# Kernel tuning notes

Measured on AMD Instinct MI355X. Metric: run time of the kernel, lower is better.

Reference implementation:

```python
import jax, jax.numpy as jnp
import numpy as np

SEQ, BATCH, IN_DIM, HID = 1024, 256, 256, 256


def setup_inputs() -> dict:
    key = jax.random.key(0)
    ks = jax.random.split(key, 9)
    s = 1.0 / np.sqrt(IN_DIM + HID)
    inp = {
        "inputs": jax.random.normal(ks[0], (SEQ, BATCH, IN_DIM), dtype=jnp.float32),
        "h0": jnp.zeros((BATCH, HID), dtype=jnp.float32),
        "c0": jnp.zeros((BATCH, HID), dtype=jnp.float32),
        # torch nn.Linear weights: [out, in] with y = x @ W.T + b
        "Wf": jax.random.uniform(ks[1], (HID, IN_DIM + HID), jnp.float32, -s, s),
        "bf": jax.random.uniform(ks[2], (HID,), jnp.float32, -s, s),
        "Wi": jax.random.uniform(ks[3], (HID, IN_DIM + HID), jnp.float32, -s, s),
        "bi": jax.random.uniform(ks[4], (HID,), jnp.float32, -s, s),
        "Wg": jax.random.uniform(ks[5], (HID, IN_DIM + HID), jnp.float32, -s, s),
        "bg": jax.random.uniform(ks[6], (HID,), jnp.float32, -s, s),
        "Wo": jax.random.uniform(ks[7], (HID, IN_DIM + HID), jnp.float32, -s, s),
        "bo": jax.random.uniform(ks[8], (HID,), jnp.float32, -s, s),
    }
    return inp


def reference(inputs, h0, c0, Wf, bf, Wi, bi, Wg, bg, Wo, bo):
    # inputs: [S, B, I]; recurrence over S via lax.scan
    def step(carry, x):
        hx, cx = carry
        combined = jnp.concatenate([x, hx], axis=1)  # [B, I+H]
        f = jax.nn.sigmoid(combined @ Wf.T + bf)
        i = jax.nn.sigmoid(combined @ Wi.T + bi)
        g = jnp.tanh(combined @ Wg.T + bg)
        o = jax.nn.sigmoid(combined @ Wo.T + bo)
        cx = f * cx + i * g
        hx = o * jnp.tanh(cx)
        return (hx, cx), hx

    (hx, cx), stacked = jax.lax.scan(step, (h0, c0), inputs)
    return stacked, (hx, cx)
```

## Files before the change

### kernel.cpp

```cpp
#include <hip/hip_runtime.h>
#include <hip/hip_bf16.h>
#include <math.h>

#define SEQ   1024
#define BATCH 256
#define IND   256
#define HID   256
#define NGATE 4

#define WB_BYTES   (2 * NGATE * HID * 256 * 2)
#define REG_BYTES  512

typedef float  f32x4  __attribute__((ext_vector_type(4)));
typedef short  bf16x8 __attribute__((ext_vector_type(8)));
typedef unsigned long long u64;

__device__ __forceinline__ short f2bf(float x) {
    __hip_bfloat16 h = __float2bfloat16(x);
    return *reinterpret_cast<short*>(&h);
}

__device__ __forceinline__ bf16x8 pack8(const float4& a, const float4& b) {
    union { short sh[8]; bf16x8 v; } u;
    u.sh[0] = f2bf(a.x); u.sh[1] = f2bf(a.y); u.sh[2] = f2bf(a.z); u.sh[3] = f2bf(a.w);
    u.sh[4] = f2bf(b.x); u.sh[5] = f2bf(b.y); u.sh[6] = f2bf(b.z); u.sh[7] = f2bf(b.w);
    return u.v;
}

__device__ __forceinline__ void gload_lds16(const void* g, void* l) {
    __builtin_amdgcn_global_load_lds(
        (const __attribute__((address_space(1))) unsigned int*)g,
        (__attribute__((address_space(3))) unsigned int*)l, 16, 0, 0);
}

__device__ __forceinline__ float sigmoid_f(float z) {
    return 1.f / (1.f + __expf(-z));
}
__device__ __forceinline__ float tanh_f(float v) {
    return 2.f / (1.f + __expf(-2.f * v)) - 1.f;
}

__device__ __forceinline__ bool stamp_ok(u64 q0, u64 q1, u64 ee) {
    return ((((q0 ^ ee) | (q1 ^ ee)) & 1ULL) == 0ULL);
}


__global__ __launch_bounds__(256) void prep_w(
    const float* __restrict__ Wf, const float* __restrict__ Wi,
    const float* __restrict__ Wg, const float* __restrict__ Wo,
    unsigned char* __restrict__ wb)
{
    int chunk = blockIdx.x * 256 + threadIdx.x;
    int g  = chunk >> 14;
    int jj = (chunk >> 6) & 255;
    int k0 = (chunk & 63) * 8;
    int p  = k0 >> 8;
    int kk = k0 & 255;
    const float* W = (g == 0) ? Wf : (g == 1) ? Wi : (g == 2) ? Wg : Wo;
    const float* src = W + (size_t)jj * 512 + k0;
    float4 a = *reinterpret_cast<const float4*>(src);
    float4 b = *reinterpret_cast<const float4*>(src + 4);
    size_t dstrow = (size_t)((p * 4 + g) * 256 + jj);
    *reinterpret_cast<bf16x8*>(
        wb + dstrow * 512 + ((kk * 2) ^ ((jj & 7) << 4))) = pack8(a, b);
}

__global__ __launch_bounds__(256) void prep_h0(
    const float* __restrict__ h0, unsigned char* __restrict__ hr)
{
    int idx  = blockIdx.x * 256 + threadIdx.x;
    int slot = idx >> 14;
    int g    = (idx >> 10) & 15;
    int J    = (idx >> 6) & 15;
    int c    = idx & 63;
    int br   = c >> 2;
    int j4   = (c & 3) * 4;
    const float* src = h0 + (size_t)(g * 16 + br) * HID + J * 16 + j4;
    unsigned short v[4];
    #pragma unroll
    for (int i = 0; i < 4; ++i)
        v[i] = (unsigned short)((unsigned short)f2bf(src[i]) | 1u);
    u64 q = (u64)v[0] | ((u64)v[1] << 16) | ((u64)v[2] << 32) | ((u64)v[3] << 48);
    *reinterpret_cast<u64*>(
        hr + (size_t)((slot * 16 + g) * 16 + J) * REG_BYTES + c * 8) = q;
}

__global__ __launch_bounds__(64, 1) void lstm_seq(
    const float* __restrict__ x,  const float* __restrict__ c0,
    const float* __restrict__ bf_, const float* __restrict__ bi_,
    const float* __restrict__ bg_, const float* __restrict__ bo_,
    const unsigned char* __restrict__ wb, unsigned char* __restrict__ hr,
    float* __restrict__ out, float* __restrict__ hx, float* __restrict__ cxg)
{
    extern __shared__ __align__(16) unsigned char smem[];

    const int lane = threadIdx.x & 63;
    const int blk  = blockIdx.x;
    const int g_   = blk & 15;
    const int J    = blk >> 4;
    const int j0   = J * 16;
    const int b0   = g_ * 16;

    const int lrow = lane & 15;
    const int hi   = lane >> 4;
    const int j    = j0 + lrow;

    #pragma unroll
    for (int i = 0; i < 64; ++i) {
        gload_lds16(wb + ((size_t)((i >> 3) * 256 + j0 + (i & 7) * 2)) * 512
                       + lane * 16,
                    smem + i * 1024);
    }
    const float biasF = bf_[j], biasI = bi_[j], biasG = bg_[j], biasO = bo_[j];
    float cst[4];
    #pragma unroll
    for (int r = 0; r < 4; ++r)
        cst[r] = c0[(b0 + hi * 4 + r) * HID + j];
    __syncthreads();

    const int bswz = (lrow & 7) << 4;
    bf16x8 wf[2][8][4];
    #pragma unroll
    for (int p = 0; p < 2; ++p) {
        #pragma unroll
        for (int kc = 0; kc < 8; ++kc) {
            int wbyte = (kc * 64 + hi * 16) ^ bswz;
            #pragma unroll
            for (int gg = 0; gg < 4; ++gg)
                wf[p][kc][gg] = *reinterpret_cast<const bf16x8*>(
                    smem + p * 32768 + gg * 8192 + lrow * 512 + wbyte);
        }
    }

    float4 xt0[8], xt1[8];
    bf16x8 xpk[8];
    {
        const float* xr = x + (size_t)(b0 + lrow) * IND;
        #pragma unroll
        for (int kc = 0; kc < 8; ++kc) {
            const float* p = xr + kc * 32 + hi * 8;
            xt0[kc] = *reinterpret_cast<const float4*>(p);
            xt1[kc] = *reinterpret_cast<const float4*>(p + 4);
        }
        #pragma unroll
        for (int kc = 0; kc < 8; ++kc) xpk[kc] = pack8(xt0[kc], xt1[kc]);
        const float* xr1 = x + ((size_t)BATCH + b0 + lrow) * IND;
        #pragma unroll
        for (int kc = 0; kc < 8; ++kc) {
            const float* p = xr1 + kc * 32 + hi * 8;
            xt0[kc] = *reinterpret_cast<const float4*>(p);
            xt1[kc] = *reinterpret_cast<const float4*>(p + 4);
        }
    }

    unsigned char* regc[2] = {
        hr + (size_t)((0 * 16 + g_) * 16) * REG_BYTES,
        hr + (size_t)((1 * 16 + g_) * 16) * REG_BYTES };
    unsigned char* regp[2] = { regc[0] + J * REG_BYTES, regc[1] + J * REG_BYTES };

    for (int s = 0; s < SEQ; ++s) {
        const u64 ee = (u64)(((unsigned)(s + 3) >> 1) & 1);
        const unsigned char* hsrc = regc[s & 1];

        u64 hq0[8], hq1[8];
        #pragma unroll
        for (int kc = 0; kc < 8; ++kc) {
            const u64* p = reinterpret_cast<const u64*>(
                hsrc + (2 * kc + (hi >> 1)) * REG_BYTES + lrow * 32 + (hi & 1) * 16);
            hq0[kc] = __hip_atomic_load(p,     __ATOMIC_RELAXED, __HIP_MEMORY_SCOPE_AGENT);
            hq1[kc] = __hip_atomic_load(p + 1, __ATOMIC_RELAXED, __HIP_MEMORY_SCOPE_AGENT);
        }
        __builtin_amdgcn_sched_barrier(0);

        f32x4 aF = {0.f, 0.f, 0.f, 0.f};
        f32x4 aI = {0.f, 0.f, 0.f, 0.f};
        f32x4 aG = {0.f, 0.f, 0.f, 0.f};
        f32x4 aO = {0.f, 0.f, 0.f, 0.f};
        #pragma unroll
        for (int kc = 0; kc < 8; ++kc) {
            aF = __builtin_amdgcn_mfma_f32_16x16x32_bf16(xpk[kc], wf[0][kc][0], aF, 0, 0, 0);
            aI = __builtin_amdgcn_mfma_f32_16x16x32_bf16(xpk[kc], wf[0][kc][1], aI, 0, 0, 0);
            aG = __builtin_amdgcn_mfma_f32_16x16x32_bf16(xpk[kc], wf[0][kc][2], aG, 0, 0, 0);
            aO = __builtin_amdgcn_mfma_f32_16x16x32_bf16(xpk[kc], wf[0][kc][3], aO, 0, 0, 0);
        }

        #pragma unroll
        for (int kc = 0; kc < 8; ++kc) xpk[kc] = pack8(xt0[kc], xt1[kc]);
        if (s + 2 < SEQ) {
            const float* xr = x + ((size_t)(s + 2) * BATCH + b0 + lrow) * IND;
            #pragma unroll
            for (int kc = 0; kc < 8; ++kc) {
                const float* p = xr + kc * 32 + hi * 8;
                xt0[kc] = *reinterpret_cast<const float4*>(p);
                xt1[kc] = *reinterpret_cast<const float4*>(p + 4);
            }
        }
        __builtin_amdgcn_sched_barrier(0);

        #pragma unroll
        for (int half = 0; half < 2; ++half) {
            const int kb = half * 4;
            unsigned pend = 0;
            #pragma unroll
            for (int kc = 0; kc < 4; ++kc)
                if (!stamp_ok(hq0[kb + kc], hq1[kb + kc], ee)) pend |= (1u << kc);
            while (pend) {
                #pragma unroll
                for (int kc = 0; kc < 4; ++kc) {
                    if (pend & (1u << kc)) {
                        const u64* p = reinterpret_cast<const u64*>(
                            hsrc + (2 * (kb + kc) + (hi >> 1)) * REG_BYTES
                                 + lrow * 32 + (hi & 1) * 16);
                        hq0[kb + kc] = __hip_atomic_load(p,     __ATOMIC_RELAXED, __HIP_MEMORY_SCOPE_AGENT);
                        hq1[kb + kc] = __hip_atomic_load(p + 1, __ATOMIC_RELAXED, __HIP_MEMORY_SCOPE_AGENT);
                        if (stamp_ok(hq0[kb + kc], hq1[kb + kc], ee)) pend &= ~(1u << kc);
                    }
                }
            }
            #pragma unroll
            for (int kc = 0; kc < 4; ++kc) {
                union { u64 q[2]; bf16x8 v; } u;
                u.q[0] = hq0[kb + kc]; u.q[1] = hq1[kb + kc];
                aF = __builtin_amdgcn_mfma_f32_16x16x32_bf16(u.v, wf[1][kb + kc][0], aF, 0, 0, 0);
                aI = __builtin_amdgcn_mfma_f32_16x16x32_bf16(u.v, wf[1][kb + kc][1], aI, 0, 0, 0);
                aG = __builtin_amdgcn_mfma_f32_16x16x32_bf16(u.v, wf[1][kb + kc][2], aG, 0, 0, 0);
                aO = __builtin_amdgcn_mfma_f32_16x16x32_bf16(u.v, wf[1][kb + kc][3], aO, 0, 0, 0);
            }
        }

        float hv[4];
        #pragma unroll
        for (int r = 0; r < 4; ++r) {
            float fg = sigmoid_f(aF[r] + biasF);
            float ig = sigmoid_f(aI[r] + biasI);
            float gg = tanh_f(aG[r] + biasG);
            float og = sigmoid_f(aO[r] + biasO);
            cst[r] = fg * cst[r] + ig * gg;
            hv[r]  = og * tanh_f(cst[r]);
        }
        #pragma unroll
        for (int r = 0; r < 4; ++r) {
            int bl = hi * 4 + r;
            *reinterpret_cast<short*>(smem + bl * 32 + lrow * 2) = f2bf(hv[r]);
            *reinterpret_cast<float*>(smem + 512 + bl * 64 + lrow * 4) = hv[r];
        }
        __builtin_amdgcn_sched_barrier(0);
        asm volatile("s_waitcnt lgkmcnt(0)" ::: "memory");
        __builtin_amdgcn_sched_barrier(0);

        {
            u64 w = *reinterpret_cast<const u64*>(smem + lane * 8);
            w = (w & ~1ULL) | (u64)((s >> 1) & 1);
            __hip_atomic_store(
                reinterpret_cast<u64*>(regp[(s + 1) & 1] + lane * 8),
                w, __ATOMIC_RELAXED, __HIP_MEMORY_SCOPE_AGENT);
        }
        {
            float4 ov = *reinterpret_cast<const float4*>(smem + 512 + lane * 16);
            *reinterpret_cast<float4*>(
                out + (size_t)s * (BATCH * HID)
                    + (size_t)(b0 + (lane >> 2)) * HID + j0 + (lane & 3) * 4) = ov;
        }
        if (s == SEQ - 1) {
            #pragma unroll
            for (int r = 0; r < 4; ++r) {
                int gi = (b0 + hi * 4 + r) * HID + j;
                hx[gi] = hv[r]; cxg[gi] = cst[r];
            }
        }
    }
}

extern "C" void kernel_launch(void* const* d_in, const int* in_sizes, int n_in,
                              void* d_out, int out_size, void* d_ws, size_t ws_size,
                              hipStream_t stream) {
    const float* x  = (const float*)d_in[0];
    const float* h0 = (const float*)d_in[1];
    const float* c0 = (const float*)d_in[2];
    const float* Wf = (const float*)d_in[3];
    const float* bf = (const float*)d_in[4];
    const float* Wi = (const float*)d_in[5];
    const float* bi = (const float*)d_in[6];
    const float* Wg = (const float*)d_in[7];
    const float* bg = (const float*)d_in[8];
    const float* Wo = (const float*)d_in[9];
    const float* bo = (const float*)d_in[10];

    float* out = (float*)d_out;
    float* hx  = out + (size_t)SEQ * BATCH * HID;
    float* cx  = hx + BATCH * HID;

    unsigned char* wb = (unsigned char*)d_ws;
    unsigned char* hr = wb + WB_BYTES;

    prep_w<<<256, 256, 0, stream>>>(Wf, Wi, Wg, Wo, wb);
    prep_h0<<<128, 256, 0, stream>>>(h0, hr);
    lstm_seq<<<256, 64, 65536, stream>>>(x, c0, bf, bi, bg, bo,
                                         wb, hr, out, hx, cx);
}
```

Baseline: 2.502 ms.

## Add producer wavefront that polls remote h state into LDS for compute wave

Adds a second wavefront per block that spins on the global stamped h buffers and copies validated chunks into a double-buffered LDS region, then signals the compute wave with an LDS flag. The compute wave now waits on the local flag and reads h from LDS instead of polling global memory itself, and it defers the fp32 output store by one step so that store overlaps the next step's work. It also raises the compute wave's priority. This is meant to take global polling latency off the critical recurrence path. The cost is an extra wave per CU and an LDS-flag handoff that relies on volatile ordering without a barrier.

```diff
diff --git a/kernel.cpp b/kernel.cpp
--- a/kernel.cpp
+++ b/kernel.cpp
@@ -10,6 +10,11 @@
 
 #define WB_BYTES   (2 * NGATE * HID * 256 * 2)
 #define REG_BYTES  512
+
+#define HBUF_OFF   0
+#define FLAG_OFF   16384
+#define HST_OFF    16448
+#define OST_OFF    17024
 
 typedef float  f32x4  __attribute__((ext_vector_type(4)));
 typedef short  bf16x8 __attribute__((ext_vector_type(8)));
@@ -85,7 +90,7 @@
         hr + (size_t)((slot * 16 + g) * 16 + J) * REG_BYTES + c * 8) = q;
 }
 
-__global__ __launch_bounds__(64, 1) void lstm_seq(
+__global__ __launch_bounds__(128, 1) void lstm_seq(
     const float* __restrict__ x,  const float* __restrict__ c0,
     const float* __restrict__ bf_, const float* __restrict__ bi_,
     const float* __restrict__ bg_, const float* __restrict__ bo_,
@@ -94,7 +99,9 @@
 {
     extern __shared__ __align__(16) unsigned char smem[];
 
-    const int lane = threadIdx.x & 63;
+    const int tid  = threadIdx.x;
+    const int lane = tid & 63;
+    const int w    = tid >> 6;
     const int blk  = blockIdx.x;
     const int g_   = blk & 15;
     const int J    = blk >> 4;
@@ -106,31 +113,87 @@
     const int j    = j0 + lrow;
 
     #pragma unroll
-    for (int i = 0; i < 64; ++i) {
-        gload_lds16(wb + ((size_t)((i >> 3) * 256 + j0 + (i & 7) * 2)) * 512
+    for (int i = 0; i < 32; ++i) {
+        int idx = w * 32 + i;
+        gload_lds16(wb + ((size_t)((idx >> 3) * 256 + j0 + (idx & 7) * 2)) * 512
                        + lane * 16,
-                    smem + i * 1024);
-    }
+                    smem + idx * 1024);
+    }
+    __syncthreads();
+
+    const int bswz = (lrow & 7) << 4;
+    bf16x8 wf[2][8][4];
+    if (w == 0) {
+        #pragma unroll
+        for (int p = 0; p < 2; ++p) {
+            #pragma unroll
+            for (int kc = 0; kc < 8; ++kc) {
+                int wbyte = (kc * 64 + hi * 16) ^ bswz;
+                #pragma unroll
+                for (int gg = 0; gg < 4; ++gg)
+                    wf[p][kc][gg] = *reinterpret_cast<const bf16x8*>(
+                        smem + p * 32768 + gg * 8192 + lrow * 512 + wbyte);
+            }
+        }
+    }
+    __syncthreads();
+    if (tid == 0) *(volatile int*)(smem + FLAG_OFF) = 0;
+    __syncthreads();
+
+    unsigned char* regc[2] = {
+        hr + (size_t)((0 * 16 + g_) * 16) * REG_BYTES,
+        hr + (size_t)((1 * 16 + g_) * 16) * REG_BYTES };
+
+    if (w == 1) {
+        for (int s = 0; s < SEQ; ++s) {
+            const u64 ee = (u64)(((unsigned)(s + 3) >> 1) & 1);
+            const unsigned char* hsrc = regc[s & 1];
+            unsigned char* dst = smem + HBUF_OFF + (s & 1) * 8192 + lane * 16;
+
+            u64 qa0[8], qa1[8];
+            #pragma unroll
+            for (int kc = 0; kc < 8; ++kc) {
+                const u64* p = reinterpret_cast<const u64*>(
+                    hsrc + (2 * kc + (hi >> 1)) * REG_BYTES + lrow * 32 + (hi & 1) * 16);
+                qa0[kc] = __hip_atomic_load(p,     __ATOMIC_RELAXED, __HIP_MEMORY_SCOPE_AGENT);
+                qa1[kc] = __hip_atomic_load(p + 1, __ATOMIC_RELAXED, __HIP_MEMORY_SCOPE_AGENT);
+            }
+            unsigned done = 0;
+            while (done != 0xffu) {
+                u64 qb0[8], qb1[8];
+                #pragma unroll
+                for (int kc = 0; kc < 8; ++kc) {
+                    const u64* p = reinterpret_cast<const u64*>(
+                        hsrc + (2 * kc + (hi >> 1)) * REG_BYTES + lrow * 32 + (hi & 1) * 16);
+                    qb0[kc] = __hip_atomic_load(p,     __ATOMIC_RELAXED, __HIP_MEMORY_SCOPE_AGENT);
+                    qb1[kc] = __hip_atomic_load(p + 1, __ATOMIC_RELAXED, __HIP_MEMORY_SCOPE_AGENT);
+                }
+                #pragma unroll
+                for (int kc = 0; kc < 8; ++kc) {
+                    if (!((done >> kc) & 1) && stamp_ok(qa0[kc], qa1[kc], ee)) {
+                        union { u64 q[2]; bf16x8 v; } u;
+                        u.q[0] = qa0[kc]; u.q[1] = qa1[kc];
+                        *reinterpret_cast<bf16x8*>(dst + kc * 1024) = u.v;
+                        done |= (1u << kc);
+                    }
+                }
+                #pragma unroll
+                for (int kc = 0; kc < 8; ++kc) { qa0[kc] = qb0[kc]; qa1[kc] = qb1[kc]; }
+            }
+            __builtin_amdgcn_sched_barrier(0);
+            asm volatile("s_waitcnt lgkmcnt(0)" ::: "memory");
+            if (lane == 0) *(volatile int*)(smem + FLAG_OFF) = s + 1;
+        }
+        return;
+    }
+
+    __builtin_amdgcn_s_setprio(1);
+
     const float biasF = bf_[j], biasI = bi_[j], biasG = bg_[j], biasO = bo_[j];
     float cst[4];
     #pragma unroll
     for (int r = 0; r < 4; ++r)
         cst[r] = c0[(b0 + hi * 4 + r) * HID + j];
-    __syncthreads();
-
-    const int bswz = (lrow & 7) << 4;
-    bf16x8 wf[2][8][4];
-    #pragma unroll
-    for (int p = 0; p < 2; ++p) {
-        #pragma unroll
-        for (int kc = 0; kc < 8; ++kc) {
-            int wbyte = (kc * 64 + hi * 16) ^ bswz;
-            #pragma unroll
-            for (int gg = 0; gg < 4; ++gg)
-                wf[p][kc][gg] = *reinterpret_cast<const bf16x8*>(
-                    smem + p * 32768 + gg * 8192 + lrow * 512 + wbyte);
-        }
-    }
 
     float4 xt0[8], xt1[8];
     bf16x8 xpk[8];
@@ -153,25 +216,11 @@
         }
     }
 
-    unsigned char* regc[2] = {
-        hr + (size_t)((0 * 16 + g_) * 16) * REG_BYTES,
-        hr + (size_t)((1 * 16 + g_) * 16) * REG_BYTES };
     unsigned char* regp[2] = { regc[0] + J * REG_BYTES, regc[1] + J * REG_BYTES };
+    volatile int* flg = (volatile int*)(smem + FLAG_OFF);
+    float hvprev[4] = {0.f, 0.f, 0.f, 0.f};
 
     for (int s = 0; s < SEQ; ++s) {
-        const u64 ee = (u64)(((unsigned)(s + 3) >> 1) & 1);
-        const unsigned char* hsrc = regc[s & 1];
-
-        u64 hq0[8], hq1[8];
-        #pragma unroll
-        for (int kc = 0; kc < 8; ++kc) {
-            const u64* p = reinterpret_cast<const u64*>(
-                hsrc + (2 * kc + (hi >> 1)) * REG_BYTES + lrow * 32 + (hi & 1) * 16);
-            hq0[kc] = __hip_atomic_load(p,     __ATOMIC_RELAXED, __HIP_MEMORY_SCOPE_AGENT);
-            hq1[kc] = __hip_atomic_load(p + 1, __ATOMIC_RELAXED, __HIP_MEMORY_SCOPE_AGENT);
-        }
-        __builtin_amdgcn_sched_barrier(0);
-
         f32x4 aF = {0.f, 0.f, 0.f, 0.f};
         f32x4 aI = {0.f, 0.f, 0.f, 0.f};
         f32x4 aG = {0.f, 0.f, 0.f, 0.f};
@@ -195,37 +244,28 @@
                 xt1[kc] = *reinterpret_cast<const float4*>(p + 4);
             }
         }
+        if (s > 0) {
+            #pragma unroll
+            for (int r = 0; r < 4; ++r)
+                *reinterpret_cast<float*>(
+                    smem + OST_OFF + (hi * 4 + r) * 64 + lrow * 4) = hvprev[r];
+            float4 ov = *reinterpret_cast<const float4*>(smem + OST_OFF + lane * 16);
+            *reinterpret_cast<float4*>(
+                out + (size_t)(s - 1) * (BATCH * HID)
+                    + (size_t)(b0 + (lane >> 2)) * HID + j0 + (lane & 3) * 4) = ov;
+        }
         __builtin_amdgcn_sched_barrier(0);
 
-        #pragma unroll
-        for (int half = 0; half < 2; ++half) {
-            const int kb = half * 4;
-            unsigned pend = 0;
-            #pragma unroll
-            for (int kc = 0; kc < 4; ++kc)
-                if (!stamp_ok(hq0[kb + kc], hq1[kb + kc], ee)) pend |= (1u << kc);
-            while (pend) {
-                #pragma unroll
-                for (int kc = 0; kc < 4; ++kc) {
-                    if (pend & (1u << kc)) {
-                        const u64* p = reinterpret_cast<const u64*>(
-                            hsrc + (2 * (kb + kc) + (hi >> 1)) * REG_BYTES
-                                 + lrow * 32 + (hi & 1) * 16);
-                        hq0[kb + kc] = __hip_atomic_load(p,     __ATOMIC_RELAXED, __HIP_MEMORY_SCOPE_AGENT);
-                        hq1[kb + kc] = __hip_atomic_load(p + 1, __ATOMIC_RELAXED, __HIP_MEMORY_SCOPE_AGENT);
-                        if (stamp_ok(hq0[kb + kc], hq1[kb + kc], ee)) pend &= ~(1u << kc);
-                    }
-                }
-            }
-            #pragma unroll
-            for (int kc = 0; kc < 4; ++kc) {
-                union { u64 q[2]; bf16x8 v; } u;
-                u.q[0] = hq0[kb + kc]; u.q[1] = hq1[kb + kc];
-                aF = __builtin_amdgcn_mfma_f32_16x16x32_bf16(u.v, wf[1][kb + kc][0], aF, 0, 0, 0);
-                aI = __builtin_amdgcn_mfma_f32_16x16x32_bf16(u.v, wf[1][kb + kc][1], aI, 0, 0, 0);
-                aG = __builtin_amdgcn_mfma_f32_16x16x32_bf16(u.v, wf[1][kb + kc][2], aG, 0, 0, 0);
-                aO = __builtin_amdgcn_mfma_f32_16x16x32_bf16(u.v, wf[1][kb + kc][3], aO, 0, 0, 0);
-            }
+        while (*flg < s + 1) {}
+        __builtin_amdgcn_sched_barrier(0);
+        const unsigned char* hb = smem + HBUF_OFF + (s & 1) * 8192;
+        #pragma unroll
+        for (int kc = 0; kc < 8; ++kc) {
+            bf16x8 hf = *reinterpret_cast<const bf16x8*>(hb + kc * 1024 + lane * 16);
+            aF = __builtin_amdgcn_mfma_f32_16x16x32_bf16(hf, wf[1][kc][0], aF, 0, 0, 0);
+            aI = __builtin_amdgcn_mfma_f32_16x16x32_bf16(hf, wf[1][kc][1], aI, 0, 0, 0);
+            aG = __builtin_amdgcn_mfma_f32_16x16x32_bf16(hf, wf[1][kc][2], aG, 0, 0, 0);
+            aO = __builtin_amdgcn_mfma_f32_16x16x32_bf16(hf, wf[1][kc][3], aO, 0, 0, 0);
         }
 
         float hv[4];
@@ -238,30 +278,31 @@
             cst[r] = fg * cst[r] + ig * gg;
             hv[r]  = og * tanh_f(cst[r]);
         }
-        #pragma unroll
-        for (int r = 0; r < 4; ++r) {
-            int bl = hi * 4 + r;
-            *reinterpret_cast<short*>(smem + bl * 32 + lrow * 2) = f2bf(hv[r]);
-            *reinterpret_cast<float*>(smem + 512 + bl * 64 + lrow * 4) = hv[r];
-        }
-        __builtin_amdgcn_sched_barrier(0);
-        asm volatile("s_waitcnt lgkmcnt(0)" ::: "memory");
-        __builtin_amdgcn_sched_barrier(0);
-
+
+        #pragma unroll
+        for (int r = 0; r < 4; ++r)
+            *reinterpret_cast<short*>(
+                smem + HST_OFF + (hi * 4 + r) * 32 + lrow * 2) = f2bf(hv[r]);
         {
-            u64 w = *reinterpret_cast<const u64*>(smem + lane * 8);
-            w = (w & ~1ULL) | (u64)((s >> 1) & 1);
+            u64 wv = *reinterpret_cast<const u64*>(smem + HST_OFF + lane * 8);
+            wv = (wv & ~1ULL) | (u64)((s >> 1) & 1);
             __hip_atomic_store(
                 reinterpret_cast<u64*>(regp[(s + 1) & 1] + lane * 8),
-                w, __ATOMIC_RELAXED, __HIP_MEMORY_SCOPE_AGENT);
-        }
-        {
-            float4 ov = *reinterpret_cast<const float4*>(smem + 512 + lane * 16);
+                wv, __ATOMIC_RELAXED, __HIP_MEMORY_SCOPE_AGENT);
+        }
+
+        #pragma unroll
+        for (int r = 0; r < 4; ++r) hvprev[r] = hv[r];
+
+        if (s == SEQ - 1) {
+            #pragma unroll
+            for (int r = 0; r < 4; ++r)
+                *reinterpret_cast<float*>(
+                    smem + OST_OFF + (hi * 4 + r) * 64 + lrow * 4) = hv[r];
+            float4 ov = *reinterpret_cast<const float4*>(smem + OST_OFF + lane * 16);
             *reinterpret_cast<float4*>(
                 out + (size_t)s * (BATCH * HID)
                     + (size_t)(b0 + (lane >> 2)) * HID + j0 + (lane & 3) * 4) = ov;
-        }
-        if (s == SEQ - 1) {
             #pragma unroll
             for (int r = 0; r < 4; ++r) {
                 int gi = (b0 + hi * 4 + r) * HID + j;
@@ -295,6 +336,6 @@
 
     prep_w<<<256, 256, 0, stream>>>(Wf, Wi, Wg, Wo, wb);
     prep_h0<<<128, 256, 0, stream>>>(h0, hr);
-    lstm_seq<<<256, 64, 65536, stream>>>(x, c0, bf, bi, bg, bo,
-                                         wb, hr, out, hx, cx);
-}
+    lstm_seq<<<256, 128, 65536, stream>>>(x, c0, bf, bi, bg, bo,
+                                          wb, hr, out, hx, cx);
+}
```

Measured after the change: 3.390 ms. +35.5%, slower.

## Add duplicate hidden-state buffer polled with sc0 loads and defer x prefetch

Applied to the files above, without the earlier changes.

Each step now writes the hidden-state exchange data to a second buffer with a volatile store, alongside the existing agent-scope atomic store. The spin-wait reads that buffer with 16-byte global loads marked sc0, falling back to the atomic buffer every eighth round. The goal is a cheaper poll with lower latency, since one wide load replaces two atomic loads per chunk. The prefetch of x for step s+2 also moves after the recurrent MFMAs, so those loads no longer compete with the poll. In exchange the code issues extra stores each step, and it relies on sc0 load coherence across CUs for correctness.

```diff
diff --git a/kernel.cpp b/kernel.cpp
--- a/kernel.cpp
+++ b/kernel.cpp
@@ -9,10 +9,12 @@
 #define NGATE 4
 
 #define WB_BYTES   (2 * NGATE * HID * 256 * 2)
+#define HR_BYTES   (2 * 16 * 16 * 512)
 #define REG_BYTES  512
 
-typedef float  f32x4  __attribute__((ext_vector_type(4)));
-typedef short  bf16x8 __attribute__((ext_vector_type(8)));
+typedef float        f32x4  __attribute__((ext_vector_type(4)));
+typedef short        bf16x8 __attribute__((ext_vector_type(8)));
+typedef unsigned int u32x4  __attribute__((ext_vector_type(4)));
 typedef unsigned long long u64;
 
 __device__ __forceinline__ short f2bf(float x) {
@@ -42,6 +44,12 @@
 
 __device__ __forceinline__ bool stamp_ok(u64 q0, u64 q1, u64 ee) {
     return ((((q0 ^ ee) | (q1 ^ ee)) & 1ULL) == 0ULL);
+}
+
+__device__ __forceinline__ u32x4 load16_sc0(const void* p) {
+    u32x4 v;
+    asm volatile("global_load_dwordx4 %0, %1, off sc0" : "=v"(v) : "v"(p));
+    return v;
 }
 
 
@@ -66,7 +74,8 @@
 }
 
 __global__ __launch_bounds__(256) void prep_h0(
-    const float* __restrict__ h0, unsigned char* __restrict__ hr)
+    const float* __restrict__ h0, unsigned char* __restrict__ hr,
+    unsigned char* __restrict__ hfast)
 {
     int idx  = blockIdx.x * 256 + threadIdx.x;
     int slot = idx >> 14;
@@ -81,8 +90,9 @@
     for (int i = 0; i < 4; ++i)
         v[i] = (unsigned short)((unsigned short)f2bf(src[i]) | 1u);
     u64 q = (u64)v[0] | ((u64)v[1] << 16) | ((u64)v[2] << 32) | ((u64)v[3] << 48);
-    *reinterpret_cast<u64*>(
-        hr + (size_t)((slot * 16 + g) * 16 + J) * REG_BYTES + c * 8) = q;
+    size_t off = (size_t)((slot * 16 + g) * 16 + J) * REG_BYTES + c * 8;
+    *reinterpret_cast<u64*>(hr + off)    = q;
+    *reinterpret_cast<u64*>(hfast + off) = q;
 }
 
 __global__ __launch_bounds__(64, 1) void lstm_seq(
@@ -90,6 +100,7 @@
     const float* __restrict__ bf_, const float* __restrict__ bi_,
     const float* __restrict__ bg_, const float* __restrict__ bo_,
     const unsigned char* __restrict__ wb, unsigned char* __restrict__ hr,
+    unsigned char* __restrict__ hfast,
     float* __restrict__ out, float* __restrict__ hx, float* __restrict__ cxg)
 {
     extern __shared__ __align__(16) unsigned char smem[];
@@ -156,17 +167,23 @@
     unsigned char* regc[2] = {
         hr + (size_t)((0 * 16 + g_) * 16) * REG_BYTES,
         hr + (size_t)((1 * 16 + g_) * 16) * REG_BYTES };
+    unsigned char* fstc[2] = {
+        hfast + (size_t)((0 * 16 + g_) * 16) * REG_BYTES,
+        hfast + (size_t)((1 * 16 + g_) * 16) * REG_BYTES };
     unsigned char* regp[2] = { regc[0] + J * REG_BYTES, regc[1] + J * REG_BYTES };
+    unsigned char* fstp[2] = { fstc[0] + J * REG_BYTES, fstc[1] + J * REG_BYTES };
 
     for (int s = 0; s < SEQ; ++s) {
         const u64 ee = (u64)(((unsigned)(s + 3) >> 1) & 1);
         const unsigned char* hsrc = regc[s & 1];
+        const unsigned char* fsrc = fstc[s & 1];
+        const int uoff = lrow * 32 + (hi & 1) * 16;
 
         u64 hq0[8], hq1[8];
         #pragma unroll
         for (int kc = 0; kc < 8; ++kc) {
             const u64* p = reinterpret_cast<const u64*>(
-                hsrc + (2 * kc + (hi >> 1)) * REG_BYTES + lrow * 32 + (hi & 1) * 16);
+                hsrc + (2 * kc + (hi >> 1)) * REG_BYTES + uoff);
             hq0[kc] = __hip_atomic_load(p,     __ATOMIC_RELAXED, __HIP_MEMORY_SCOPE_AGENT);
             hq1[kc] = __hip_atomic_load(p + 1, __ATOMIC_RELAXED, __HIP_MEMORY_SCOPE_AGENT);
         }
@@ -183,18 +200,8 @@
             aG = __builtin_amdgcn_mfma_f32_16x16x32_bf16(xpk[kc], wf[0][kc][2], aG, 0, 0, 0);
             aO = __builtin_amdgcn_mfma_f32_16x16x32_bf16(xpk[kc], wf[0][kc][3], aO, 0, 0, 0);
         }
-
         #pragma unroll
         for (int kc = 0; kc < 8; ++kc) xpk[kc] = pack8(xt0[kc], xt1[kc]);
-        if (s + 2 < SEQ) {
-            const float* xr = x + ((size_t)(s + 2) * BATCH + b0 + lrow) * IND;
-            #pragma unroll
-            for (int kc = 0; kc < 8; ++kc) {
-                const float* p = xr + kc * 32 + hi * 8;
-                xt0[kc] = *reinterpret_cast<const float4*>(p);
-                xt1[kc] = *reinterpret_cast<const float4*>(p + 4);
-            }
-        }
         __builtin_amdgcn_sched_barrier(0);
 
         #pragma unroll
@@ -204,18 +211,40 @@
             #pragma unroll
             for (int kc = 0; kc < 4; ++kc)
                 if (!stamp_ok(hq0[kb + kc], hq1[kb + kc], ee)) pend |= (1u << kc);
+            int round = 0;
             while (pend) {
-                #pragma unroll
-                for (int kc = 0; kc < 4; ++kc) {
-                    if (pend & (1u << kc)) {
-                        const u64* p = reinterpret_cast<const u64*>(
-                            hsrc + (2 * (kb + kc) + (hi >> 1)) * REG_BYTES
-                                 + lrow * 32 + (hi & 1) * 16);
-                        hq0[kb + kc] = __hip_atomic_load(p,     __ATOMIC_RELAXED, __HIP_MEMORY_SCOPE_AGENT);
-                        hq1[kb + kc] = __hip_atomic_load(p + 1, __ATOMIC_RELAXED, __HIP_MEMORY_SCOPE_AGENT);
-                        if (stamp_ok(hq0[kb + kc], hq1[kb + kc], ee)) pend &= ~(1u << kc);
+                if ((round & 7) == 7) {
+                    #pragma unroll
+                    for (int kc = 0; kc < 4; ++kc) {
+                        if (pend & (1u << kc)) {
+                            const u64* p = reinterpret_cast<const u64*>(
+                                hsrc + (2 * (kb + kc) + (hi >> 1)) * REG_BYTES + uoff);
+                            hq0[kb + kc] = __hip_atomic_load(p,     __ATOMIC_RELAXED, __HIP_MEMORY_SCOPE_AGENT);
+                            hq1[kb + kc] = __hip_atomic_load(p + 1, __ATOMIC_RELAXED, __HIP_MEMORY_SCOPE_AGENT);
+                        }
+                    }
+                } else {
+                    u32x4 pv[4];
+                    #pragma unroll
+                    for (int kc = 0; kc < 4; ++kc)
+                        if (pend & (1u << kc))
+                            pv[kc] = load16_sc0(
+                                fsrc + (2 * (kb + kc) + (hi >> 1)) * REG_BYTES + uoff);
+                    asm volatile("s_waitcnt vmcnt(0)" ::: "memory");
+                    __builtin_amdgcn_sched_barrier(0);
+                    #pragma unroll
+                    for (int kc = 0; kc < 4; ++kc) {
+                        if (pend & (1u << kc)) {
+                            hq0[kb + kc] = (u64)pv[kc].x | ((u64)pv[kc].y << 32);
+                            hq1[kb + kc] = (u64)pv[kc].z | ((u64)pv[kc].w << 32);
+                        }
                     }
                 }
+                #pragma unroll
+                for (int kc = 0; kc < 4; ++kc)
+                    if ((pend & (1u << kc)) &&
+                        stamp_ok(hq0[kb + kc], hq1[kb + kc], ee)) pend &= ~(1u << kc);
+                ++round;
             }
             #pragma unroll
             for (int kc = 0; kc < 4; ++kc) {
@@ -228,6 +257,16 @@
             }
         }
 
+        if (s + 2 < SEQ) {
+            const float* xr = x + ((size_t)(s + 2) * BATCH + b0 + lrow) * IND;
+            #pragma unroll
+            for (int kc = 0; kc < 8; ++kc) {
+                const float* p = xr + kc * 32 + hi * 8;
+                xt0[kc] = *reinterpret_cast<const float4*>(p);
+                xt1[kc] = *reinterpret_cast<const float4*>(p + 4);
+            }
+        }
+
         float hv[4];
         #pragma unroll
         for (int r = 0; r < 4; ++r) {
@@ -249,11 +288,12 @@
         __builtin_amdgcn_sched_barrier(0);
 
         {
-            u64 w = *reinterpret_cast<const u64*>(smem + lane * 8);
-            w = (w & ~1ULL) | (u64)((s >> 1) & 1);
+            u64 wv = *reinterpret_cast<const u64*>(smem + lane * 8);
+            wv = (wv & ~1ULL) | (u64)((s >> 1) & 1);
+            *reinterpret_cast<volatile u64*>(fstp[(s + 1) & 1] + lane * 8) = wv;
             __hip_atomic_store(
                 reinterpret_cast<u64*>(regp[(s + 1) & 1] + lane * 8),
-                w, __ATOMIC_RELAXED, __HIP_MEMORY_SCOPE_AGENT);
+                wv, __ATOMIC_RELAXED, __HIP_MEMORY_SCOPE_AGENT);
         }
         {
             float4 ov = *reinterpret_cast<const float4*>(smem + 512 + lane * 16);
@@ -292,9 +332,10 @@
 
     unsigned char* wb = (unsigned char*)d_ws;
     unsigned char* hr = wb + WB_BYTES;
+    unsigned char* hf = hr + HR_BYTES;
 
     prep_w<<<256, 256, 0, stream>>>(Wf, Wi, Wg, Wo, wb);
-    prep_h0<<<128, 256, 0, stream>>>(h0, hr);
+    prep_h0<<<128, 256, 0, stream>>>(h0, hr, hf);
     lstm_seq<<<256, 64, 65536, stream>>>(x, c0, bf, bi, bg, bo,
-                                         wb, hr, out, hx, cx);
-}
+                                         wb, hr, hf, out, hx, cx);
+}
```

After: 3.673 ms. 46.8% more time.

## Transpose MFMA operands, stream input weights from LDS, pipeline h polling

Applied to the files above, without the earlier changes.

Swaps the MFMA operand order so that each lane owns four consecutive hidden units for one batch row. This lets the bf16 h publish and the fp32 output store go straight from registers, removing the LDS staging round-trip and its lgkmcnt wait. Input-projection weights are now re-read from LDS every step instead of being held in registers, which frees VGPRs. The h-polling uses inline-asm sc0 sc1 loads that are double-buffered: a second probe is issued before the previous one is checked, aiming to hide flag-spin latency. The cost is extra LDS traffic per step and redundant global probes, and correctness now depends on the hand-written vmcnt accounting.

```diff
diff --git a/kernel.cpp b/kernel.cpp
--- a/kernel.cpp
+++ b/kernel.cpp
@@ -42,6 +42,12 @@
 
 __device__ __forceinline__ bool stamp_ok(u64 q0, u64 q1, u64 ee) {
     return ((((q0 ^ ee) | (q1 ^ ee)) & 1ULL) == 0ULL);
+}
+
+__device__ __forceinline__ void probe2(const void* p, u64& q0, u64& q1) {
+    asm volatile("global_load_dwordx2 %0, %2, off sc0 sc1\n\t"
+                 "global_load_dwordx2 %1, %2, off offset:8 sc0 sc1"
+                 : "=&v"(q0), "=&v"(q1) : "v"(p));
 }
 
 
@@ -103,7 +109,8 @@
 
     const int lrow = lane & 15;
     const int hi   = lane >> 4;
-    const int j    = j0 + lrow;
+    const int b    = b0 + lrow;
+    const int jv   = j0 + hi * 4;
 
     #pragma unroll
     for (int i = 0; i < 64; ++i) {
@@ -111,31 +118,28 @@
                        + lane * 16,
                     smem + i * 1024);
     }
-    const float biasF = bf_[j], biasI = bi_[j], biasG = bg_[j], biasO = bo_[j];
-    float cst[4];
+    const float4 biasF4 = *reinterpret_cast<const float4*>(bf_ + jv);
+    const float4 biasI4 = *reinterpret_cast<const float4*>(bi_ + jv);
+    const float4 biasG4 = *reinterpret_cast<const float4*>(bg_ + jv);
+    const float4 biasO4 = *reinterpret_cast<const float4*>(bo_ + jv);
+    float4 cst = *reinterpret_cast<const float4*>(c0 + (size_t)b * HID + jv);
+    __syncthreads();
+
+    const int bswz = (lrow & 7) << 4;
+    bf16x8 wfh[8][4];
     #pragma unroll
-    for (int r = 0; r < 4; ++r)
-        cst[r] = c0[(b0 + hi * 4 + r) * HID + j];
-    __syncthreads();
-
-    const int bswz = (lrow & 7) << 4;
-    bf16x8 wf[2][8][4];
-    #pragma unroll
-    for (int p = 0; p < 2; ++p) {
-        #pragma unroll
-        for (int kc = 0; kc < 8; ++kc) {
-            int wbyte = (kc * 64 + hi * 16) ^ bswz;
-            #pragma unroll
-            for (int gg = 0; gg < 4; ++gg)
-                wf[p][kc][gg] = *reinterpret_cast<const bf16x8*>(
-                    smem + p * 32768 + gg * 8192 + lrow * 512 + wbyte);
-        }
+    for (int kc = 0; kc < 8; ++kc) {
+        int wbyte = (kc * 64 + hi * 16) ^ bswz;
+        #pragma unroll
+        for (int gg = 0; gg < 4; ++gg)
+            wfh[kc][gg] = *reinterpret_cast<const bf16x8*>(
+                smem + 32768 + gg * 8192 + lrow * 512 + wbyte);
     }
 
     float4 xt0[8], xt1[8];
     bf16x8 xpk[8];
     {
-        const float* xr = x + (size_t)(b0 + lrow) * IND;
+        const float* xr = x + (size_t)b * IND;
         #pragma unroll
         for (int kc = 0; kc < 8; ++kc) {
             const float* p = xr + kc * 32 + hi * 8;
@@ -144,7 +148,7 @@
         }
         #pragma unroll
         for (int kc = 0; kc < 8; ++kc) xpk[kc] = pack8(xt0[kc], xt1[kc]);
-        const float* xr1 = x + ((size_t)BATCH + b0 + lrow) * IND;
+        const float* xr1 = x + ((size_t)BATCH + b) * IND;
         #pragma unroll
         for (int kc = 0; kc < 8; ++kc) {
             const float* p = xr1 + kc * 32 + hi * 8;
@@ -157,19 +161,17 @@
         hr + (size_t)((0 * 16 + g_) * 16) * REG_BYTES,
         hr + (size_t)((1 * 16 + g_) * 16) * REG_BYTES };
     unsigned char* regp[2] = { regc[0] + J * REG_BYTES, regc[1] + J * REG_BYTES };
+    const int uoff = lrow * 32 + (hi & 1) * 16;
 
     for (int s = 0; s < SEQ; ++s) {
         const u64 ee = (u64)(((unsigned)(s + 3) >> 1) & 1);
         const unsigned char* hsrc = regc[s & 1];
 
-        u64 hq0[8], hq1[8];
-        #pragma unroll
-        for (int kc = 0; kc < 8; ++kc) {
-            const u64* p = reinterpret_cast<const u64*>(
-                hsrc + (2 * kc + (hi >> 1)) * REG_BYTES + lrow * 32 + (hi & 1) * 16);
-            hq0[kc] = __hip_atomic_load(p,     __ATOMIC_RELAXED, __HIP_MEMORY_SCOPE_AGENT);
-            hq1[kc] = __hip_atomic_load(p + 1, __ATOMIC_RELAXED, __HIP_MEMORY_SCOPE_AGENT);
-        }
+        u64 qa0[8], qa1[8], qb0[8], qb1[8];
+        #pragma unroll
+        for (int kc = 0; kc < 8; ++kc)
+            probe2(hsrc + (2 * kc + (hi >> 1)) * REG_BYTES + uoff,
+                   qa0[kc], qa1[kc]);
         __builtin_amdgcn_sched_barrier(0);
 
         f32x4 aF = {0.f, 0.f, 0.f, 0.f};
@@ -178,16 +180,78 @@
         f32x4 aO = {0.f, 0.f, 0.f, 0.f};
         #pragma unroll
         for (int kc = 0; kc < 8; ++kc) {
-            aF = __builtin_amdgcn_mfma_f32_16x16x32_bf16(xpk[kc], wf[0][kc][0], aF, 0, 0, 0);
-            aI = __builtin_amdgcn_mfma_f32_16x16x32_bf16(xpk[kc], wf[0][kc][1], aI, 0, 0, 0);
-            aG = __builtin_amdgcn_mfma_f32_16x16x32_bf16(xpk[kc], wf[0][kc][2], aG, 0, 0, 0);
-            aO = __builtin_amdgcn_mfma_f32_16x16x32_bf16(xpk[kc], wf[0][kc][3], aO, 0, 0, 0);
-        }
-
+            int wbyte = (kc * 64 + hi * 16) ^ bswz;
+            const unsigned char* wr = smem + lrow * 512 + wbyte;
+            bf16x8 vF = *reinterpret_cast<const bf16x8*>(wr);
+            bf16x8 vI = *reinterpret_cast<const bf16x8*>(wr + 8192);
+            bf16x8 vG = *reinterpret_cast<const bf16x8*>(wr + 16384);
+            bf16x8 vO = *reinterpret_cast<const bf16x8*>(wr + 24576);
+            aF = __builtin_amdgcn_mfma_f32_16x16x32_bf16(vF, xpk[kc], aF, 0, 0, 0);
+            aI = __builtin_amdgcn_mfma_f32_16x16x32_bf16(vI, xpk[kc], aI, 0, 0, 0);
+            aG = __builtin_amdgcn_mfma_f32_16x16x32_bf16(vG, xpk[kc], aG, 0, 0, 0);
+            aO = __builtin_amdgcn_mfma_f32_16x16x32_bf16(vO, xpk[kc], aO, 0, 0, 0);
+        }
         #pragma unroll
         for (int kc = 0; kc < 8; ++kc) xpk[kc] = pack8(xt0[kc], xt1[kc]);
+        __builtin_amdgcn_sched_barrier(0);
+
+        unsigned pend = 0xffu;
+        while (pend) {
+            #pragma unroll
+            for (int kc = 0; kc < 8; ++kc)
+                probe2(hsrc + (2 * kc + (hi >> 1)) * REG_BYTES + uoff,
+                       qb0[kc], qb1[kc]);
+            asm volatile("s_waitcnt vmcnt(16)" ::: "memory");
+            __builtin_amdgcn_sched_barrier(0);
+            #pragma unroll
+            for (int kc = 0; kc < 8; ++kc)
+                if ((pend & (1u << kc)) && stamp_ok(qa0[kc], qa1[kc], ee))
+                    pend &= ~(1u << kc);
+            if (pend) {
+                #pragma unroll
+                for (int kc = 0; kc < 8; ++kc) { qa0[kc] = qb0[kc]; qa1[kc] = qb1[kc]; }
+            }
+        }
+        __builtin_amdgcn_sched_barrier(0);
+
+        #pragma unroll
+        for (int kc = 0; kc < 8; ++kc) {
+            union { u64 q[2]; bf16x8 v; } u;
+            u.q[0] = qa0[kc]; u.q[1] = qa1[kc];
+            aF = __builtin_amdgcn_mfma_f32_16x16x32_bf16(wfh[kc][0], u.v, aF, 0, 0, 0);
+            aI = __builtin_amdgcn_mfma_f32_16x16x32_bf16(wfh[kc][1], u.v, aI, 0, 0, 0);
+            aG = __builtin_amdgcn_mfma_f32_16x16x32_bf16(wfh[kc][2], u.v, aG, 0, 0, 0);
+            aO = __builtin_amdgcn_mfma_f32_16x16x32_bf16(wfh[kc][3], u.v, aO, 0, 0, 0);
+        }
+
+        float hv[4];
+        #pragma unroll
+        for (int r = 0; r < 4; ++r) {
+            float fg = sigmoid_f(aF[r] + ((const float*)&biasF4)[r]);
+            float ig = sigmoid_f(aI[r] + ((const float*)&biasI4)[r]);
+            float gg = tanh_f(aG[r] + ((const float*)&biasG4)[r]);
+            float og = sigmoid_f(aO[r] + ((const float*)&biasO4)[r]);
+            ((float*)&cst)[r] = fg * ((const float*)&cst)[r] + ig * gg;
+            hv[r] = og * tanh_f(((const float*)&cst)[r]);
+        }
+
+        {
+            u64 wv = (u64)(unsigned short)f2bf(hv[0])
+                   | ((u64)(unsigned short)f2bf(hv[1]) << 16)
+                   | ((u64)(unsigned short)f2bf(hv[2]) << 32)
+                   | ((u64)(unsigned short)f2bf(hv[3]) << 48);
+            wv = (wv & ~1ULL) | (u64)((s >> 1) & 1);
+            __hip_atomic_store(
+                reinterpret_cast<u64*>(regp[(s + 1) & 1] + lrow * 32 + hi * 8),
+                wv, __ATOMIC_RELAXED, __HIP_MEMORY_SCOPE_AGENT);
+        }
+        {
+            float4 ov = { hv[0], hv[1], hv[2], hv[3] };
+            *reinterpret_cast<float4*>(
+                out + (size_t)s * (BATCH * HID) + (size_t)b * HID + jv) = ov;
+        }
         if (s + 2 < SEQ) {
-            const float* xr = x + ((size_t)(s + 2) * BATCH + b0 + lrow) * IND;
+            const float* xr = x + ((size_t)(s + 2) * BATCH + b) * IND;
             #pragma unroll
             for (int kc = 0; kc < 8; ++kc) {
                 const float* p = xr + kc * 32 + hi * 8;
@@ -195,79 +259,16 @@
                 xt1[kc] = *reinterpret_cast<const float4*>(p + 4);
             }
         }
-        __builtin_amdgcn_sched_barrier(0);
-
-        #pragma unroll
-        for (int half = 0; half < 2; ++half) {
-            const int kb = half * 4;
-            unsigned pend = 0;
-            #pragma unroll
-            for (int kc = 0; kc < 4; ++kc)
-                if (!stamp_ok(hq0[kb + kc], hq1[kb + kc], ee)) pend |= (1u << kc);
-            while (pend) {
-                #pragma unroll
-                for (int kc = 0; kc < 4; ++kc) {
-                    if (pend & (1u << kc)) {
-                        const u64* p = reinterpret_cast<const u64*>(
-                            hsrc + (2 * (kb + kc) + (hi >> 1)) * REG_BYTES
-                                 + lrow * 32 + (hi & 1) * 16);
-                        hq0[kb + kc] = __hip_atomic_load(p,     __ATOMIC_RELAXED, __HIP_MEMORY_SCOPE_AGENT);
-                        hq1[kb + kc] = __hip_atomic_load(p + 1, __ATOMIC_RELAXED, __HIP_MEMORY_SCOPE_AGENT);
-                        if (stamp_ok(hq0[kb + kc], hq1[kb + kc], ee)) pend &= ~(1u << kc);
-                    }
-                }
-            }
-            #pragma unroll
-            for (int kc = 0; kc < 4; ++kc) {
-                union { u64 q[2]; bf16x8 v; } u;
-                u.q[0] = hq0[kb + kc]; u.q[1] = hq1[kb + kc];
-                aF = __builtin_amdgcn_mfma_f32_16x16x32_bf16(u.v, wf[1][kb + kc][0], aF, 0, 0, 0);
-                aI = __builtin_amdgcn_mfma_f32_16x16x32_bf16(u.v, wf[1][kb + kc][1], aI, 0, 0, 0);
-                aG = __builtin_amdgcn_mfma_f32_16x16x32_bf16(u.v, wf[1][kb + kc][2], aG, 0, 0, 0);
-                aO = __builtin_amdgcn_mfma_f32_16x16x32_bf16(u.v, wf[1][kb + kc][3], aO, 0, 0, 0);
-            }
-        }
-
-        float hv[4];
-        #pragma unroll
-        for (int r = 0; r < 4; ++r) {
-            float fg = sigmoid_f(aF[r] + biasF);
-            float ig = sigmoid_f(aI[r] + biasI);
-            float gg = tanh_f(aG[r] + biasG);
-            float og = sigmoid_f(aO[r] + biasO);
-            cst[r] = fg * cst[r] + ig * gg;
-            hv[r]  = og * tanh_f(cst[r]);
-        }
-        #pragma unroll
-        for (int r = 0; r < 4; ++r) {
-            int bl = hi * 4 + r;
-            *reinterpret_cast<short*>(smem + bl * 32 + lrow * 2) = f2bf(hv[r]);
-            *reinterpret_cast<float*>(smem + 512 + bl * 64 + lrow * 4) = hv[r];
-        }
-        __builtin_amdgcn_sched_barrier(0);
-        asm volatile("s_waitcnt lgkmcnt(0)" ::: "memory");
-        __builtin_amdgcn_sched_barrier(0);
-
-        {
-            u64 w = *reinterpret_cast<const u64*>(smem + lane * 8);
-            w = (w & ~1ULL) | (u64)((s >> 1) & 1);
-            __hip_atomic_store(
-                reinterpret_cast<u64*>(regp[(s + 1) & 1] + lane * 8),
-                w, __ATOMIC_RELAXED, __HIP_MEMORY_SCOPE_AGENT);
-        }
-        {
-            float4 ov = *reinterpret_cast<const float4*>(smem + 512 + lane * 16);
-            *reinterpret_cast<float4*>(
-                out + (size_t)s * (BATCH * HID)
-                    + (size_t)(b0 + (lane >> 2)) * HID + j0 + (lane & 3) * 4) = ov;
-        }
         if (s == SEQ - 1) {
-            #pragma unroll
-            for (int r = 0; r < 4; ++r) {
-                int gi = (b0 + hi * 4 + r) * HID + j;
-                hx[gi] = hv[r]; cxg[gi] = cst[r];
-            }
-        }
+            *reinterpret_cast<float4*>(hx  + (size_t)b * HID + jv) =
+                (float4){ hv[0], hv[1], hv[2], hv[3] };
+            *reinterpret_cast<float4*>(cxg + (size_t)b * HID + jv) = cst;
+        }
+        asm volatile("" ::
+            "v"(qb0[0]), "v"(qb0[1]), "v"(qb0[2]), "v"(qb0[3]),
+            "v"(qb0[4]), "v"(qb0[5]), "v"(qb0[6]), "v"(qb0[7]),
+            "v"(qb1[0]), "v"(qb1[1]), "v"(qb1[2]), "v"(qb1[3]),
+            "v"(qb1[4]), "v"(qb1[5]), "v"(qb1[6]), "v"(qb1[7]));
     }
 }
 
```

Result: slower. 2.975 ms (+18.9%).
